# Kernel optimization log

Hardware: AMD Instinct MI355X
Metric: run time of the kernel (lower is better)

Reference implementation:

```python
import jax, jax.numpy as jnp
import numpy as np

N = 2048
DIM_A = 256   # appearance feature dim (hardcoded 256 in WK/WQ/WV)
DIM_K = 64    # key_feature_dim
DIM_G = 64    # geo_feature_dim


def setup_inputs() -> dict:
    key = jax.random.key(0)
    ks = jax.random.split(key, 12)
    s = 0.05
    return {
        "f_a": jax.random.normal(ks[0], (N, DIM_A), dtype=jnp.float32),
        "position_embedding": jax.random.normal(ks[1], (N, N, DIM_G), dtype=jnp.float32),
        # torch nn.Linear weights are [out_features, in_features]
        "WG_w": jax.random.normal(ks[2], (1, DIM_G), dtype=jnp.float32) * s,
        "WG_b": jax.random.normal(ks[3], (1,), dtype=jnp.float32) * s,
        "WK_w": jax.random.normal(ks[4], (DIM_K, DIM_A), dtype=jnp.float32) * s,
        "WK_b": jax.random.normal(ks[5], (DIM_K,), dtype=jnp.float32) * s,
        "WQ_w": jax.random.normal(ks[6], (DIM_K, DIM_A), dtype=jnp.float32) * s,
        "WQ_b": jax.random.normal(ks[7], (DIM_K,), dtype=jnp.float32) * s,
        "WV_w": jax.random.normal(ks[8], (DIM_K, DIM_A), dtype=jnp.float32) * s,
        "WV_b": jax.random.normal(ks[9], (DIM_K,), dtype=jnp.float32) * s,
    }


def reference(f_a, position_embedding, WG_w, WG_b, WK_w, WK_b, WQ_w, WQ_b, WV_w, WV_b):
    n = f_a.shape[0]
    dim_k = WK_w.shape[0]
    dim_g = WG_w.shape[1]
    # geometric bias: relu(WG(g)), then log-clamp -> [N, N]
    w_g = jax.nn.relu(position_embedding.reshape(-1, dim_g) @ WG_w.T + WG_b).reshape(n, n)
    # projections of appearance features
    w_k = f_a @ WK_w.T + WK_b   # [N, dim_k]  (key index m)
    w_q = f_a @ WQ_w.T + WQ_b   # [N, dim_k]  (query index n)
    w_v = f_a @ WV_w.T + WV_b   # [N, dim_k]
    # scaled dot product: scores[m, n] = k_m . q_n / sqrt(dim_k)
    scaled_dot = (w_k @ w_q.T) / jnp.sqrt(jnp.asarray(dim_k, dtype=f_a.dtype))
    w_mn = jnp.log(jnp.clip(w_g, 1e-6)) + scaled_dot
    w_mn = jax.nn.softmax(w_mn, axis=1)        # softmax over dim=1 as in source
    # weighted sum of values along the softmax axis -> [N, dim_k]
    output = w_mn @ w_v
    return output
```

## Files before the change

### kernel.cpp

```cpp
#include <hip/hip_runtime.h>
#include <hip/hip_bf16.h>
#include <math.h>

#define NN 2048
#define DA 256
#define DK 64
#define DG 64

typedef float f32x4 __attribute__((ext_vector_type(4)));

__device__ __forceinline__ float wave_reduce_max(float v) {
  #pragma unroll
  for (int o = 32; o >= 1; o >>= 1) v = fmaxf(v, __shfl_xor(v, o, 64));
  return v;
}
__device__ __forceinline__ float wave_reduce_sum(float v) {
  #pragma unroll
  for (int o = 32; o >= 1; o >>= 1) v += __shfl_xor(v, o, 64);
  return v;
}

__device__ __forceinline__ float dpp_reduce16(float x) {
  int t;
  t = __builtin_amdgcn_update_dpp(0, __float_as_int(x), 0xB1, 0xF, 0xF, true);
  x += __int_as_float(t);
  t = __builtin_amdgcn_update_dpp(0, __float_as_int(x), 0x4E, 0xF, 0xF, true);
  x += __int_as_float(t);
  t = __builtin_amdgcn_update_dpp(0, __float_as_int(x), 0x124, 0xF, 0xF, true);
  x += __int_as_float(t);
  t = __builtin_amdgcn_update_dpp(0, __float_as_int(x), 0x128, 0xF, 0xF, true);
  x += __int_as_float(t);
  return x;
}

__global__ __launch_bounds__(256) void proj_kernel(
    const float* __restrict__ fa,
    const float* __restrict__ WKw, const float* __restrict__ WKb,
    const float* __restrict__ WQw, const float* __restrict__ WQb,
    const float* __restrict__ WVw, const float* __restrict__ WVb,
    float* __restrict__ wk, float* __restrict__ wq, float* __restrict__ wv)
{
  __shared__ float s_fa[DA];
  const int m = blockIdx.x, tid = threadIdx.x;
  s_fa[tid] = fa[(size_t)m * DA + tid];
  __syncthreads();
  if (tid < 192) {
    const int o = tid >> 6, k = tid & 63;
    const float* W = (o == 0 ? WKw : (o == 1 ? WQw : WVw)) + (size_t)k * DA;
    const float* B = (o == 0 ? WKb : (o == 1 ? WQb : WVb));
    float acc = B[k];
    const float4* W4 = (const float4*)W;
    const float4* F4 = (const float4*)s_fa;
    #pragma unroll 8
    for (int c = 0; c < DA / 4; ++c) {
      float4 w4 = W4[c], f4 = F4[c];
      acc = fmaf(w4.x, f4.x, acc); acc = fmaf(w4.y, f4.y, acc);
      acc = fmaf(w4.z, f4.z, acc); acc = fmaf(w4.w, f4.w, acc);
    }
    float* dst = (o == 0 ? wk : (o == 1 ? wq : wv));
    dst[(size_t)m * DK + k] = acc;
  }
}

__global__ __launch_bounds__(256) void fused_kernel(
    const float* __restrict__ pe,
    const float* __restrict__ wgw, const float* __restrict__ wgb,
    const float* __restrict__ wk, const float* __restrict__ wq,
    const float* __restrict__ wv,
    float* __restrict__ out)
{
  __shared__ float s_logit[NN];
  __shared__ float s_rmax[4], s_rsum[4];
  __shared__ float s_pacc[4][4][DK];

  const int m = blockIdx.x, tid = threadIdx.x;
  const int wave = tid >> 6, lane = tid & 63;
  const int sub = lane >> 4;
  const int c4  = lane & 15;

  const f32x4 wg4 = ((const f32x4*)wgw)[c4];
  const f32x4 wk4 = ((const f32x4*)(wk + (size_t)m * DK))[c4];
  const float gb = wgb[0];

  float lmax = -INFINITY;
  const int n0 = wave * (NN / 4);
  #pragma unroll 4
  for (int it = 0; it < (NN / 4) / 4; ++it) {
    const int nb = n0 + it * 4;
    const f32x4 p = __builtin_nontemporal_load(
        (const f32x4*)(pe + ((size_t)m * NN + nb) * DG) + lane);
    const f32x4 q = ((const f32x4*)(wq + (size_t)nb * DK))[lane];
    float dg = p.x * wg4.x, dq = q.x * wk4.x;
    dg = fmaf(p.y, wg4.y, dg); dq = fmaf(q.y, wk4.y, dq);
    dg = fmaf(p.z, wg4.z, dg); dq = fmaf(q.z, wk4.z, dq);
    dg = fmaf(p.w, wg4.w, dg); dq = fmaf(q.w, wk4.w, dq);
    dg = dpp_reduce16(dg);
    dq = dpp_reduce16(dq);
    if (c4 == 0) {
      const float logit = __logf(fmaxf(dg + gb, 1e-6f)) + dq * 0.125f;
      s_logit[nb + sub] = logit;
      lmax = fmaxf(lmax, logit);
    }
  }
  lmax = wave_reduce_max(lmax);
  if (lane == 0) s_rmax[wave] = lmax;
  __syncthreads();
  const float rmax = fmaxf(fmaxf(s_rmax[0], s_rmax[1]), fmaxf(s_rmax[2], s_rmax[3]));

  float lsum = 0.f;
  #pragma unroll
  for (int i = 0; i < NN / 256; ++i) {
    const int n = i * 256 + tid;
    const float p = __expf(s_logit[n] - rmax);
    s_logit[n] = p;
    lsum += p;
  }
  lsum = wave_reduce_sum(lsum);
  if (lane == 0) s_rsum[wave] = lsum;
  __syncthreads();
  const float inv = 1.0f / (s_rsum[0] + s_rsum[1] + s_rsum[2] + s_rsum[3]);

  f32x4 acc = {0.f, 0.f, 0.f, 0.f};
  #pragma unroll 4
  for (int it = 0; it < (NN / 4) / 4; ++it) {
    const int nb = n0 + it * 4;
    const float pb = s_logit[nb + sub];
    const f32x4 v = ((const f32x4*)(wv + (size_t)(nb + sub) * DK))[c4];
    acc.x = fmaf(pb, v.x, acc.x);
    acc.y = fmaf(pb, v.y, acc.y);
    acc.z = fmaf(pb, v.z, acc.z);
    acc.w = fmaf(pb, v.w, acc.w);
  }
  ((f32x4*)&s_pacc[wave][sub][0])[c4] = acc;
  __syncthreads();
  if (tid < DK) {
    float r = 0.f;
    #pragma unroll
    for (int w = 0; w < 4; ++w)
      #pragma unroll
      for (int s = 0; s < 4; ++s)
        r += s_pacc[w][s][tid];
    out[(size_t)m * DK + tid] = r * inv;
  }
}

extern "C" void kernel_launch(void* const* d_in, const int* in_sizes, int n_in,
                              void* d_out, int out_size, void* d_ws, size_t ws_size,
                              hipStream_t stream) {
  const float* fa  = (const float*)d_in[0];
  const float* pe  = (const float*)d_in[1];
  const float* wgw = (const float*)d_in[2];
  const float* wgb = (const float*)d_in[3];
  const float* wkw = (const float*)d_in[4];
  const float* wkb = (const float*)d_in[5];
  const float* wqw = (const float*)d_in[6];
  const float* wqb = (const float*)d_in[7];
  const float* wvw = (const float*)d_in[8];
  const float* wvb = (const float*)d_in[9];
  float* out = (float*)d_out;

  float* wk = (float*)d_ws;
  float* wq = wk + (size_t)NN * DK;
  float* wv = wq + (size_t)NN * DK;

  proj_kernel<<<NN, 256, 0, stream>>>(fa, wkw, wkb, wqw, wqb, wvw, wvb, wk, wq, wv);
  fused_kernel<<<NN, 256, 0, stream>>>(pe, wgw, wgb, wk, wq, wv, out);
}
```

Baseline: 267.9 us.

## Fuse softmax and value accumulation into a single online-softmax pass

Replaces the three-phase softmax (write logits to LDS, compute max, exponentiate and sum, then a second loop over V) with one streaming pass. Each lane keeps a running max, sum and value accumulator, and wave and block partials are merged with rescaling. This removes the LDS logit buffer, two block barriers and the second sweep over wv. In exchange every lane now computes two exps and a log per iteration instead of only one lane in sixteen, and the unroll factor is reduced.

```diff
diff --git a/kernel.cpp b/kernel.cpp
--- a/kernel.cpp
+++ b/kernel.cpp
@@ -8,17 +8,6 @@
 #define DG 64
 
 typedef float f32x4 __attribute__((ext_vector_type(4)));
-
-__device__ __forceinline__ float wave_reduce_max(float v) {
-  #pragma unroll
-  for (int o = 32; o >= 1; o >>= 1) v = fmaxf(v, __shfl_xor(v, o, 64));
-  return v;
-}
-__device__ __forceinline__ float wave_reduce_sum(float v) {
-  #pragma unroll
-  for (int o = 32; o >= 1; o >>= 1) v += __shfl_xor(v, o, 64);
-  return v;
-}
 
 __device__ __forceinline__ float dpp_reduce16(float x) {
   int t;
@@ -69,9 +58,8 @@
     const float* __restrict__ wv,
     float* __restrict__ out)
 {
-  __shared__ float s_logit[NN];
-  __shared__ float s_rmax[4], s_rsum[4];
-  __shared__ float s_pacc[4][4][DK];
+  __shared__ float s_wacc[4][DK];
+  __shared__ float s_wm[4], s_wl[4];
 
   const int m = blockIdx.x, tid = threadIdx.x;
   const int wave = tid >> 6, lane = tid & 63;
@@ -82,65 +70,66 @@
   const f32x4 wk4 = ((const f32x4*)(wk + (size_t)m * DK))[c4];
   const float gb = wgb[0];
 
-  float lmax = -INFINITY;
+  float om = -INFINITY;
+  float ol = 0.f;
+  f32x4 acc = {0.f, 0.f, 0.f, 0.f};
+
   const int n0 = wave * (NN / 4);
-  #pragma unroll 4
+  #pragma unroll 2
   for (int it = 0; it < (NN / 4) / 4; ++it) {
     const int nb = n0 + it * 4;
     const f32x4 p = __builtin_nontemporal_load(
         (const f32x4*)(pe + ((size_t)m * NN + nb) * DG) + lane);
     const f32x4 q = ((const f32x4*)(wq + (size_t)nb * DK))[lane];
+    const f32x4 v = ((const f32x4*)(wv + (size_t)(nb + sub) * DK))[c4];
+
     float dg = p.x * wg4.x, dq = q.x * wk4.x;
     dg = fmaf(p.y, wg4.y, dg); dq = fmaf(q.y, wk4.y, dq);
     dg = fmaf(p.z, wg4.z, dg); dq = fmaf(q.z, wk4.z, dq);
     dg = fmaf(p.w, wg4.w, dg); dq = fmaf(q.w, wk4.w, dq);
     dg = dpp_reduce16(dg);
     dq = dpp_reduce16(dq);
-    if (c4 == 0) {
-      const float logit = __logf(fmaxf(dg + gb, 1e-6f)) + dq * 0.125f;
-      s_logit[nb + sub] = logit;
-      lmax = fmaxf(lmax, logit);
+
+    const float logit = __logf(fmaxf(dg + gb, 1e-6f)) + dq * 0.125f;
+
+    const float mn = fmaxf(om, logit);
+    const float scale = __expf(om - mn);
+    const float pr = __expf(logit - mn);
+    ol = fmaf(ol, scale, pr);
+    acc.x = fmaf(acc.x, scale, pr * v.x);
+    acc.y = fmaf(acc.y, scale, pr * v.y);
+    acc.z = fmaf(acc.z, scale, pr * v.z);
+    acc.w = fmaf(acc.w, scale, pr * v.w);
+    om = mn;
+  }
+
+  float M = fmaxf(om, __shfl_xor(om, 16, 64));
+  M = fmaxf(M, __shfl_xor(M, 32, 64));
+  const float f = __expf(om - M);
+  ol *= f;
+  acc.x *= f; acc.y *= f; acc.z *= f; acc.w *= f;
+  ol    += __shfl_xor(ol, 16, 64);    ol    += __shfl_xor(ol, 32, 64);
+  acc.x += __shfl_xor(acc.x, 16, 64); acc.x += __shfl_xor(acc.x, 32, 64);
+  acc.y += __shfl_xor(acc.y, 16, 64); acc.y += __shfl_xor(acc.y, 32, 64);
+  acc.z += __shfl_xor(acc.z, 16, 64); acc.z += __shfl_xor(acc.z, 32, 64);
+  acc.w += __shfl_xor(acc.w, 16, 64); acc.w += __shfl_xor(acc.w, 32, 64);
+
+  if (lane < 16) {
+    ((f32x4*)s_wacc[wave])[lane] = acc;
+    if (lane == 0) { s_wm[wave] = M; s_wl[wave] = ol; }
+  }
+  __syncthreads();
+
+  if (tid < DK) {
+    const float Mg = fmaxf(fmaxf(s_wm[0], s_wm[1]), fmaxf(s_wm[2], s_wm[3]));
+    float L = 0.f, r = 0.f;
+    #pragma unroll
+    for (int w = 0; w < 4; ++w) {
+      const float fw = __expf(s_wm[w] - Mg);
+      L = fmaf(s_wl[w], fw, L);
+      r = fmaf(s_wacc[w][tid], fw, r);
     }
-  }
-  lmax = wave_reduce_max(lmax);
-  if (lane == 0) s_rmax[wave] = lmax;
-  __syncthreads();
-  const float rmax = fmaxf(fmaxf(s_rmax[0], s_rmax[1]), fmaxf(s_rmax[2], s_rmax[3]));
-
-  float lsum = 0.f;
-  #pragma unroll
-  for (int i = 0; i < NN / 256; ++i) {
-    const int n = i * 256 + tid;
-    const float p = __expf(s_logit[n] - rmax);
-    s_logit[n] = p;
-    lsum += p;
-  }
-  lsum = wave_reduce_sum(lsum);
-  if (lane == 0) s_rsum[wave] = lsum;
-  __syncthreads();
-  const float inv = 1.0f / (s_rsum[0] + s_rsum[1] + s_rsum[2] + s_rsum[3]);
-
-  f32x4 acc = {0.f, 0.f, 0.f, 0.f};
-  #pragma unroll 4
-  for (int it = 0; it < (NN / 4) / 4; ++it) {
-    const int nb = n0 + it * 4;
-    const float pb = s_logit[nb + sub];
-    const f32x4 v = ((const f32x4*)(wv + (size_t)(nb + sub) * DK))[c4];
-    acc.x = fmaf(pb, v.x, acc.x);
-    acc.y = fmaf(pb, v.y, acc.y);
-    acc.z = fmaf(pb, v.z, acc.z);
-    acc.w = fmaf(pb, v.w, acc.w);
-  }
-  ((f32x4*)&s_pacc[wave][sub][0])[c4] = acc;
-  __syncthreads();
-  if (tid < DK) {
-    float r = 0.f;
-    #pragma unroll
-    for (int w = 0; w < 4; ++w)
-      #pragma unroll
-      for (int s = 0; s < 4; ++s)
-        r += s_pacc[w][s][tid];
-    out[(size_t)m * DK + tid] = r * inv;
+    out[(size_t)m * DK + tid] = r / L;
   }
 }
 
```

Result: slower. 284.3 us (+6.1%).

## Process four query rows per block and precompute QK scores tile-wise

Applied to the files above, without the earlier changes.

Each block of the fused kernel now handles four rows m instead of one. The full Q·K score rows for those four rows are computed first into shared memory, reusing each wq load across all four rows. The position-embedding stream then adds the log-clamped geometric bias in place, and the softmax and V accumulation reuse each wv load across the four rows. This amortizes the repeated wq/wv traffic that every row used to reload. In exchange the grid has 4x fewer blocks, each using more LDS and registers, which lowers occupancy for the bandwidth-bound stream over the position embeddings.

```diff
diff --git a/kernel.cpp b/kernel.cpp
--- a/kernel.cpp
+++ b/kernel.cpp
@@ -6,6 +6,7 @@
 #define DA 256
 #define DK 64
 #define DG 64
+#define MROWS 4
 
 typedef float f32x4 __attribute__((ext_vector_type(4)));
 
@@ -31,6 +32,14 @@
   t = __builtin_amdgcn_update_dpp(0, __float_as_int(x), 0x128, 0xF, 0xF, true);
   x += __int_as_float(t);
   return x;
+}
+
+__device__ __forceinline__ float dot4(const f32x4 a, const f32x4 b) {
+  float d = a.x * b.x;
+  d = fmaf(a.y, b.y, d);
+  d = fmaf(a.z, b.z, d);
+  d = fmaf(a.w, b.w, d);
+  return d;
 }
 
 __global__ __launch_bounds__(256) void proj_kernel(
@@ -69,78 +78,125 @@
     const float* __restrict__ wv,
     float* __restrict__ out)
 {
-  __shared__ float s_logit[NN];
-  __shared__ float s_rmax[4], s_rsum[4];
-  __shared__ float s_pacc[4][4][DK];
-
-  const int m = blockIdx.x, tid = threadIdx.x;
+  __shared__ float s_sc[MROWS][NN];
+  __shared__ float s_pacc[4][MROWS][DK];
+  __shared__ float s_rsum[MROWS];
+
+  const int m0 = blockIdx.x * MROWS;
+  const int tid = threadIdx.x;
   const int wave = tid >> 6, lane = tid & 63;
   const int sub = lane >> 4;
   const int c4  = lane & 15;
 
+  {
+    float acc[8][MROWS];
+    #pragma unroll
+    for (int j = 0; j < 8; ++j)
+      #pragma unroll
+      for (int i = 0; i < MROWS; ++i) acc[j][i] = 0.f;
+    #pragma unroll 4
+    for (int c = 0; c < DK / 4; ++c) {
+      f32x4 wkc[MROWS];
+      #pragma unroll
+      for (int i = 0; i < MROWS; ++i)
+        wkc[i] = ((const f32x4*)(wk + (size_t)(m0 + i) * DK))[c];
+      #pragma unroll
+      for (int j = 0; j < 8; ++j) {
+        const int n = j * 256 + tid;
+        const f32x4 q = ((const f32x4*)(wq + (size_t)n * DK))[c];
+        #pragma unroll
+        for (int i = 0; i < MROWS; ++i) {
+          acc[j][i] = fmaf(q.x, wkc[i].x, acc[j][i]);
+          acc[j][i] = fmaf(q.y, wkc[i].y, acc[j][i]);
+          acc[j][i] = fmaf(q.z, wkc[i].z, acc[j][i]);
+          acc[j][i] = fmaf(q.w, wkc[i].w, acc[j][i]);
+        }
+      }
+    }
+    #pragma unroll
+    for (int j = 0; j < 8; ++j) {
+      const int n = j * 256 + tid;
+      #pragma unroll
+      for (int i = 0; i < MROWS; ++i)
+        s_sc[i][n] = acc[j][i] * 0.125f;
+    }
+  }
+  __syncthreads();
+
   const f32x4 wg4 = ((const f32x4*)wgw)[c4];
-  const f32x4 wk4 = ((const f32x4*)(wk + (size_t)m * DK))[c4];
   const float gb = wgb[0];
-
-  float lmax = -INFINITY;
-  const int n0 = wave * (NN / 4);
+  const int n0w = wave * (NN / 4);
+  #pragma unroll 2
+  for (int it = 0; it < (NN / 4) / 4; ++it) {
+    const int nb = n0w + it * 4;
+    f32x4 p[MROWS];
+    #pragma unroll
+    for (int i = 0; i < MROWS; ++i)
+      p[i] = __builtin_nontemporal_load(
+          (const f32x4*)(pe + ((size_t)(m0 + i) * NN + nb) * DG) + lane);
+    #pragma unroll
+    for (int i = 0; i < MROWS; ++i) {
+      float dg = dot4(p[i], wg4);
+      dg = dpp_reduce16(dg);
+      if (c4 == 0) {
+        s_sc[i][nb + sub] += __logf(fmaxf(dg + gb, 1e-6f));
+      }
+    }
+  }
+  __syncthreads();
+
+  {
+    float mx = -INFINITY;
+    #pragma unroll
+    for (int j = 0; j < NN / 64; ++j)
+      mx = fmaxf(mx, s_sc[wave][j * 64 + lane]);
+    mx = wave_reduce_max(mx);
+    float sm = 0.f;
+    #pragma unroll
+    for (int j = 0; j < NN / 64; ++j) {
+      const float pr = __expf(s_sc[wave][j * 64 + lane] - mx);
+      s_sc[wave][j * 64 + lane] = pr;
+      sm += pr;
+    }
+    sm = wave_reduce_sum(sm);
+    if (lane == 0) s_rsum[wave] = sm;
+  }
+  __syncthreads();
+
+  f32x4 vacc[MROWS];
+  #pragma unroll
+  for (int i = 0; i < MROWS; ++i) vacc[i] = (f32x4){0.f, 0.f, 0.f, 0.f};
   #pragma unroll 4
   for (int it = 0; it < (NN / 4) / 4; ++it) {
-    const int nb = n0 + it * 4;
-    const f32x4 p = __builtin_nontemporal_load(
-        (const f32x4*)(pe + ((size_t)m * NN + nb) * DG) + lane);
-    const f32x4 q = ((const f32x4*)(wq + (size_t)nb * DK))[lane];
-    float dg = p.x * wg4.x, dq = q.x * wk4.x;
-    dg = fmaf(p.y, wg4.y, dg); dq = fmaf(q.y, wk4.y, dq);
-    dg = fmaf(p.z, wg4.z, dg); dq = fmaf(q.z, wk4.z, dq);
-    dg = fmaf(p.w, wg4.w, dg); dq = fmaf(q.w, wk4.w, dq);
-    dg = dpp_reduce16(dg);
-    dq = dpp_reduce16(dq);
-    if (c4 == 0) {
-      const float logit = __logf(fmaxf(dg + gb, 1e-6f)) + dq * 0.125f;
-      s_logit[nb + sub] = logit;
-      lmax = fmaxf(lmax, logit);
-    }
-  }
-  lmax = wave_reduce_max(lmax);
-  if (lane == 0) s_rmax[wave] = lmax;
-  __syncthreads();
-  const float rmax = fmaxf(fmaxf(s_rmax[0], s_rmax[1]), fmaxf(s_rmax[2], s_rmax[3]));
-
-  float lsum = 0.f;
-  #pragma unroll
-  for (int i = 0; i < NN / 256; ++i) {
-    const int n = i * 256 + tid;
-    const float p = __expf(s_logit[n] - rmax);
-    s_logit[n] = p;
-    lsum += p;
-  }
-  lsum = wave_reduce_sum(lsum);
-  if (lane == 0) s_rsum[wave] = lsum;
-  __syncthreads();
-  const float inv = 1.0f / (s_rsum[0] + s_rsum[1] + s_rsum[2] + s_rsum[3]);
-
-  f32x4 acc = {0.f, 0.f, 0.f, 0.f};
-  #pragma unroll 4
-  for (int it = 0; it < (NN / 4) / 4; ++it) {
-    const int nb = n0 + it * 4;
-    const float pb = s_logit[nb + sub];
-    const f32x4 v = ((const f32x4*)(wv + (size_t)(nb + sub) * DK))[c4];
-    acc.x = fmaf(pb, v.x, acc.x);
-    acc.y = fmaf(pb, v.y, acc.y);
-    acc.z = fmaf(pb, v.z, acc.z);
-    acc.w = fmaf(pb, v.w, acc.w);
-  }
-  ((f32x4*)&s_pacc[wave][sub][0])[c4] = acc;
-  __syncthreads();
-  if (tid < DK) {
-    float r = 0.f;
-    #pragma unroll
-    for (int w = 0; w < 4; ++w)
-      #pragma unroll
-      for (int s = 0; s < 4; ++s)
-        r += s_pacc[w][s][tid];
-    out[(size_t)m * DK + tid] = r * inv;
+    const int n = n0w + it * 4 + sub;
+    const f32x4 v = ((const f32x4*)(wv + (size_t)n * DK))[c4];
+    #pragma unroll
+    for (int i = 0; i < MROWS; ++i) {
+      const float pr = s_sc[i][n];
+      vacc[i].x = fmaf(pr, v.x, vacc[i].x);
+      vacc[i].y = fmaf(pr, v.y, vacc[i].y);
+      vacc[i].z = fmaf(pr, v.z, vacc[i].z);
+      vacc[i].w = fmaf(pr, v.w, vacc[i].w);
+    }
+  }
+  #pragma unroll
+  for (int i = 0; i < MROWS; ++i) {
+    vacc[i].x += __shfl_xor(vacc[i].x, 16, 64); vacc[i].x += __shfl_xor(vacc[i].x, 32, 64);
+    vacc[i].y += __shfl_xor(vacc[i].y, 16, 64); vacc[i].y += __shfl_xor(vacc[i].y, 32, 64);
+    vacc[i].z += __shfl_xor(vacc[i].z, 16, 64); vacc[i].z += __shfl_xor(vacc[i].z, 32, 64);
+    vacc[i].w += __shfl_xor(vacc[i].w, 16, 64); vacc[i].w += __shfl_xor(vacc[i].w, 32, 64);
+  }
+  if (lane < 16) {
+    #pragma unroll
+    for (int i = 0; i < MROWS; ++i)
+      ((f32x4*)s_pacc[wave][i])[c4] = vacc[i];
+  }
+  __syncthreads();
+  {
+    const int i = tid >> 6, k = tid & 63;
+    const float r = s_pacc[0][i][k] + s_pacc[1][i][k] +
+                    s_pacc[2][i][k] + s_pacc[3][i][k];
+    out[(size_t)(m0 + i) * DK + k] = r / s_rsum[i];
   }
 }
 
@@ -164,5 +220,5 @@
   float* wv = wq + (size_t)NN * DK;
 
   proj_kernel<<<NN, 256, 0, stream>>>(fa, wkw, wkb, wqw, wqb, wvw, wvb, wk, wq, wv);
-  fused_kernel<<<NN, 256, 0, stream>>>(pe, wgw, wgb, wk, wq, wv, out);
-}
+  fused_kernel<<<NN / MROWS, 256, 0, stream>>>(pe, wgw, wgb, wk, wq, wv, out);
+}
```

Measured after the change: 280.9 us. 1.05x slower.

## Precompute K·Q scores in separate register-tiled kernel, simplify fused pass

Applied to the files above, without the earlier changes.

Moves the scaled K·Q dot products out of the fused softmax kernel into a new register-tiled scores kernel that writes a full N×N score matrix to workspace. The fused kernel then loads its score row into shared memory, adds only the log-clamped geometric bias from the streamed position embedding, and computes the max in a separate pass. The goal is to cut the per-row ALU and cross-lane reduction work in the bandwidth-bound pass. The cost is an extra 16 MB score matrix written and read back, one more kernel launch and extra block barriers. The value-accumulation unroll is also raised.

```diff
diff --git a/kernel.cpp b/kernel.cpp
--- a/kernel.cpp
+++ b/kernel.cpp
@@ -31,6 +31,14 @@
   t = __builtin_amdgcn_update_dpp(0, __float_as_int(x), 0x128, 0xF, 0xF, true);
   x += __int_as_float(t);
   return x;
+}
+
+__device__ __forceinline__ float dot4(const f32x4 a, const f32x4 b) {
+  float d = a.x * b.x;
+  d = fmaf(a.y, b.y, d);
+  d = fmaf(a.z, b.z, d);
+  d = fmaf(a.w, b.w, d);
+  return d;
 }
 
 __global__ __launch_bounds__(256) void proj_kernel(
@@ -62,11 +70,49 @@
   }
 }
 
+__global__ __launch_bounds__(256) void scores_kernel(
+    const float* __restrict__ wk, const float* __restrict__ wq,
+    float* __restrict__ S)
+{
+  const int m0 = blockIdx.x * 4;
+  const int tid = threadIdx.x;
+  float acc[8][4];
+  #pragma unroll
+  for (int j = 0; j < 8; ++j)
+    #pragma unroll
+    for (int i = 0; i < 4; ++i) acc[j][i] = 0.f;
+  #pragma unroll 4
+  for (int c = 0; c < DK / 4; ++c) {
+    f32x4 wkc[4];
+    #pragma unroll
+    for (int i = 0; i < 4; ++i)
+      wkc[i] = ((const f32x4*)(wk + (size_t)(m0 + i) * DK))[c];
+    #pragma unroll
+    for (int j = 0; j < 8; ++j) {
+      const int n = j * 256 + tid;
+      const f32x4 q = ((const f32x4*)(wq + (size_t)n * DK))[c];
+      #pragma unroll
+      for (int i = 0; i < 4; ++i) {
+        acc[j][i] = fmaf(q.x, wkc[i].x, acc[j][i]);
+        acc[j][i] = fmaf(q.y, wkc[i].y, acc[j][i]);
+        acc[j][i] = fmaf(q.z, wkc[i].z, acc[j][i]);
+        acc[j][i] = fmaf(q.w, wkc[i].w, acc[j][i]);
+      }
+    }
+  }
+  #pragma unroll
+  for (int j = 0; j < 8; ++j) {
+    const int n = j * 256 + tid;
+    #pragma unroll
+    for (int i = 0; i < 4; ++i)
+      S[(size_t)(m0 + i) * NN + n] = acc[j][i] * 0.125f;
+  }
+}
+
 __global__ __launch_bounds__(256) void fused_kernel(
     const float* __restrict__ pe,
     const float* __restrict__ wgw, const float* __restrict__ wgb,
-    const float* __restrict__ wk, const float* __restrict__ wq,
-    const float* __restrict__ wv,
+    const float* __restrict__ S, const float* __restrict__ wv,
     float* __restrict__ out)
 {
   __shared__ float s_logit[NN];
@@ -78,35 +124,39 @@
   const int sub = lane >> 4;
   const int c4  = lane & 15;
 
+  {
+    const f32x4* Sr = (const f32x4*)(S + (size_t)m * NN);
+    f32x4* L = (f32x4*)s_logit;
+    #pragma unroll
+    for (int j = 0; j < (NN / 4) / 256; ++j)
+      L[j * 256 + tid] = Sr[j * 256 + tid];
+  }
   const f32x4 wg4 = ((const f32x4*)wgw)[c4];
-  const f32x4 wk4 = ((const f32x4*)(wk + (size_t)m * DK))[c4];
   const float gb = wgb[0];
-
-  float lmax = -INFINITY;
+  __syncthreads();
+
   const int n0 = wave * (NN / 4);
   #pragma unroll 4
   for (int it = 0; it < (NN / 4) / 4; ++it) {
     const int nb = n0 + it * 4;
     const f32x4 p = __builtin_nontemporal_load(
         (const f32x4*)(pe + ((size_t)m * NN + nb) * DG) + lane);
-    const f32x4 q = ((const f32x4*)(wq + (size_t)nb * DK))[lane];
-    float dg = p.x * wg4.x, dq = q.x * wk4.x;
-    dg = fmaf(p.y, wg4.y, dg); dq = fmaf(q.y, wk4.y, dq);
-    dg = fmaf(p.z, wg4.z, dg); dq = fmaf(q.z, wk4.z, dq);
-    dg = fmaf(p.w, wg4.w, dg); dq = fmaf(q.w, wk4.w, dq);
+    float dg = dot4(p, wg4);
     dg = dpp_reduce16(dg);
-    dq = dpp_reduce16(dq);
     if (c4 == 0) {
-      const float logit = __logf(fmaxf(dg + gb, 1e-6f)) + dq * 0.125f;
-      s_logit[nb + sub] = logit;
-      lmax = fmaxf(lmax, logit);
+      s_logit[nb + sub] += __logf(fmaxf(dg + gb, 1e-6f));
     }
   }
-  lmax = wave_reduce_max(lmax);
-  if (lane == 0) s_rmax[wave] = lmax;
+  __syncthreads();
+
+  float mx = -INFINITY;
+  #pragma unroll
+  for (int i = 0; i < NN / 256; ++i)
+    mx = fmaxf(mx, s_logit[i * 256 + tid]);
+  mx = wave_reduce_max(mx);
+  if (lane == 0) s_rmax[wave] = mx;
   __syncthreads();
   const float rmax = fmaxf(fmaxf(s_rmax[0], s_rmax[1]), fmaxf(s_rmax[2], s_rmax[3]));
-
   float lsum = 0.f;
   #pragma unroll
   for (int i = 0; i < NN / 256; ++i) {
@@ -121,7 +171,7 @@
   const float inv = 1.0f / (s_rsum[0] + s_rsum[1] + s_rsum[2] + s_rsum[3]);
 
   f32x4 acc = {0.f, 0.f, 0.f, 0.f};
-  #pragma unroll 4
+  #pragma unroll 8
   for (int it = 0; it < (NN / 4) / 4; ++it) {
     const int nb = n0 + it * 4;
     const float pb = s_logit[nb + sub];
@@ -162,7 +212,9 @@
   float* wk = (float*)d_ws;
   float* wq = wk + (size_t)NN * DK;
   float* wv = wq + (size_t)NN * DK;
+  float* S  = wv + (size_t)NN * DK;
 
   proj_kernel<<<NN, 256, 0, stream>>>(fa, wkw, wkb, wqw, wqb, wvw, wvb, wk, wq, wv);
-  fused_kernel<<<NN, 256, 0, stream>>>(pe, wgw, wgb, wk, wq, wv, out);
-}
+  scores_kernel<<<NN / 4, 256, 0, stream>>>(wk, wq, S);
+  fused_kernel<<<NN, 256, 0, stream>>>(pe, wgw, wgb, S, wv, out);
+}
```

New measurement: 345.5 us. 28.9% more time.
